# Kernel tuning notes

Hardware: AMD Instinct MI355X
Metric: run time of the kernel (lower is better)

Reference implementation:

```python
import jax, jax.numpy as jnp
import numpy as np

IN_FEATURES = 4096
OUT_FEATURES = 4096
CODESZ = 4
CB_SIZE = 256


def fwht(x):
    """Fast Walsh-Hadamard transform over the last dim (power of 2), unnormalized."""
    shape = x.shape
    n = shape[-1]
    x = x.reshape(-1, n)
    h = 1
    while h < n:  # log2(n) fixed iterations
        x = x.reshape(x.shape[0], -1, 2, h)
        a = x[:, :, 0:1, :]
        b = x[:, :, 1:2, :]
        x = jnp.concatenate([a + b, a - b], axis=2)
        h *= 2
    return x.reshape(shape)


def setup_inputs() -> dict:
    key = jax.random.key(0)
    k1, k2, k3, k4, k5, k6 = jax.random.split(key, 6)
    inp = {
        "input": jax.random.normal(k1, (4, 2048, IN_FEATURES), dtype=jnp.float32),
        "SU": jax.random.uniform(k2, (IN_FEATURES,), dtype=jnp.float32),
        "SV": jax.random.uniform(k3, (OUT_FEATURES,), dtype=jnp.float32),
        "cb": jax.random.normal(k4, (CB_SIZE, CODESZ), dtype=jnp.float32),
        "Qidxs": jax.random.randint(k5, (OUT_FEATURES, IN_FEATURES // CODESZ), 0, CB_SIZE, dtype=jnp.int32),
        "Wscale": jnp.ones((1,), dtype=jnp.float32),
        "bias": jax.random.normal(k6, (OUT_FEATURES,), dtype=jnp.float32),
    }
    return inp


def reference(input, SU, SV, cb, Qidxs, Wscale, bias):
    q_in = IN_FEATURES   # power of 2 -> had_left is None, K_left = 1
    q_out = OUT_FEATURES # power of 2 -> had_right is None, K_right = 1
    x = input.reshape(-1, input.shape[-1])          # [T, in]
    x = x * SU                                       # input sign/scale vector
    # matmul_hadUt_cuda: FWHT / sqrt(n) * wscale
    x = fwht(x) * (Wscale[0] / jnp.sqrt(jnp.float32(q_in)))
    # codebook decode + matmul: W [q_out, q_in] from indices
    W = cb[Qidxs].reshape(q_out, q_in)               # gather decode
    out = jnp.einsum('ti,oi->to', x, W)              # [T, q_out]
    # matmul_hadU_cuda on the output side: FWHT / sqrt(n)
    out = fwht(out) / jnp.sqrt(jnp.float32(q_out))
    out = out[..., :OUT_FEATURES]
    out = out * SV
    out = out.reshape(*input.shape[:-1], OUT_FEATURES)
    out = out + bias
    return out
```

## Files before the change

### kernel.cpp

```cpp
#include <hip/hip_runtime.h>
#include <cstdint>


using bf16x8 = __attribute__((ext_vector_type(8))) __bf16;
using f32x4  = __attribute__((ext_vector_type(4))) float;

__device__ __forceinline__ unsigned short f2bf(float f) {
    unsigned int u = __float_as_uint(f);
    unsigned int r = (u + 0x7fffu + ((u >> 16) & 1u)) >> 16;
    return (unsigned short)r;
}

__device__ __forceinline__ void h16(float v[16]) {
#pragma unroll
    for (int h = 1; h < 16; h <<= 1) {
#pragma unroll
        for (int g = 0; g < 16; g += (h << 1)) {
#pragma unroll
            for (int k = g; k < g + h; ++k) {
                float x = v[k], y = v[k + h];
                v[k] = x + y; v[k + h] = x - y;
            }
        }
    }
}


__global__ __launch_bounds__(256) void fwht_in_kernel(const float* __restrict__ inp,
                                                      const float* __restrict__ SU,
                                                      const float* __restrict__ wscale,
                                                      unsigned short* __restrict__ X) {
    __shared__ float s[4096];
    const int t = threadIdx.x;
    const size_t base = (size_t)blockIdx.x * 4096;
    const float4* in4 = (const float4*)(inp + base);
    const float4* su4 = (const float4*)SU;
#pragma unroll
    for (int j = 0; j < 4; ++j) {
        const int v = t + (j << 8);
        float4 x = in4[v];
        float4 u = su4[v];
        x.x *= u.x; x.y *= u.y; x.z *= u.z; x.w *= u.w;
        const int a = v >> 6, b = (v >> 2) & 15, c0 = (v & 3) << 2;
        float* row = s + a * 256 + ((b ^ a) << 4);
        row[(c0 + 0) ^ b] = x.x; row[(c0 + 1) ^ b] = x.y;
        row[(c0 + 2) ^ b] = x.z; row[(c0 + 3) ^ b] = x.w;
    }
    __syncthreads();
    float v[16];
    {
        const int a = t >> 4, b = t & 15;
        float* row = s + a * 256 + ((b ^ a) << 4);
#pragma unroll
        for (int c = 0; c < 16; ++c) v[c] = row[c ^ b];
        h16(v);
#pragma unroll
        for (int c = 0; c < 16; ++c) row[c ^ b] = v[c];
    }
    __syncthreads();
    {
        const int a = t >> 4, c = t & 15;
#pragma unroll
        for (int b = 0; b < 16; ++b) v[b] = s[a * 256 + ((b ^ a) << 4) + (c ^ b)];
        h16(v);
#pragma unroll
        for (int b = 0; b < 16; ++b) s[a * 256 + ((b ^ a) << 4) + (c ^ b)] = v[b];
    }
    __syncthreads();
    {
        const int b = t >> 4, c = t & 15;
#pragma unroll
        for (int a = 0; a < 16; ++a) v[a] = s[a * 256 + ((b ^ a) << 4) + (c ^ b)];
        h16(v);
#pragma unroll
        for (int a = 0; a < 16; ++a) s[a * 256 + ((b ^ a) << 4) + (c ^ b)] = v[a];
    }
    __syncthreads();
    const float sc = wscale[0] * 0.015625f;
#pragma unroll
    for (int p = 0; p < 2; ++p) {
        const int i0 = (p << 11) + (t << 3);
        const int a = i0 >> 8, b = (i0 >> 4) & 15, c0 = i0 & 15;
        const float* row = s + a * 256 + ((b ^ a) << 4);
        union { unsigned short us[8]; uint4 q; } pk;
#pragma unroll
        for (int z = 0; z < 8; ++z) pk.us[z] = f2bf(row[(c0 + z) ^ b] * sc);
        *(uint4*)(X + base + i0) = pk.q;
    }
}

__global__ __launch_bounds__(256) void decode_kernel(const int* __restrict__ Qidxs,
                                                     const float* __restrict__ cb,
                                                     unsigned short* __restrict__ Wb) {
    __shared__ float4 cbs[256];
    const int t = threadIdx.x;
    cbs[t] = ((const float4*)cb)[t];
    __syncthreads();
    const size_t o = blockIdx.x;
    const int* q = Qidxs + o * 1024;
    ushort4* wrow = (ushort4*)(Wb + o * 4096);
#pragma unroll
    for (int jj = 0; jj < 4; ++jj) {
        int j = t + (jj << 8);
        int idx = q[j];
        float4 v = cbs[idx];
        ushort4 w4;
        w4.x = f2bf(v.x); w4.y = f2bf(v.y); w4.z = f2bf(v.z); w4.w = f2bf(v.w);
        wrow[j] = w4;
    }
}


__device__ __forceinline__ void stage_part(const unsigned short* __restrict__ src,
                                           int grow, int kt,
                                           unsigned short* dst, int tid) {
#pragma unroll
    for (int j = 0; j < 2; ++j) {
        int u = tid + j * 512;
        int r = u >> 3;
        int q = (u & 7) ^ (r & 7);
        const unsigned short* g = src + (size_t)(grow + r) * 4096 + kt + q * 8;
        __builtin_amdgcn_global_load_lds(
            (const __attribute__((address_space(1))) unsigned int*)g,
            (__attribute__((address_space(3))) unsigned int*)((char*)dst + u * 16),
            16, 0, 0);
    }
}

#define VM4 asm volatile("s_waitcnt vmcnt(4)" ::: "memory")
#define VM0 asm volatile("s_waitcnt vmcnt(0)" ::: "memory")

#define RD_A(HOFF) do { _Pragma("unroll")                                          \
    for (int m_ = 0; m_ < 4; ++m_) {                                               \
        Ak0[m_] = *(const bf16x8*)(pA_ + (HOFF) + aRow + m_ * 4096 + pu0);         \
        Ak1[m_] = *(const bf16x8*)(pA_ + (HOFF) + aRow + m_ * 4096 + pu1);         \
    } } while (0)

#define RD_B(D0, D1, HOFF) do { _Pragma("unroll")                                  \
    for (int n_ = 0; n_ < 2; ++n_) {                                               \
        D0[n_] = *(const bf16x8*)(pB_ + (HOFF) + bRow + n_ * 8192 + pu0);          \
        D1[n_] = *(const bf16x8*)(pB_ + (HOFF) + bRow + n_ * 8192 + pu1);          \
    } } while (0)

#define MMQ(MQ, NQ, Bk0, Bk1) do {                                                 \
    __builtin_amdgcn_s_setprio(1);                                                 \
    _Pragma("unroll")                                                              \
    for (int m_ = 0; m_ < 4; ++m_) { _Pragma("unroll")                             \
        for (int n_ = 0; n_ < 2; ++n_) {                                           \
            acc[(MQ)*4+m_][(NQ)*2+n_] = __builtin_amdgcn_mfma_f32_16x16x32_bf16(   \
                Ak0[m_], Bk0[n_], acc[(MQ)*4+m_][(NQ)*2+n_], 0, 0, 0);             \
            acc[(MQ)*4+m_][(NQ)*2+n_] = __builtin_amdgcn_mfma_f32_16x16x32_bf16(   \
                Ak1[m_], Bk1[n_], acc[(MQ)*4+m_][(NQ)*2+n_], 0, 0, 0);             \
        } }                                                                        \
    __builtin_amdgcn_s_setprio(0); } while (0)

#define KTILE(PA, PB, ST1, ST2, ST3, ST4, VM_) do {                                \
    const char* pA_ = (const char*)(PA);                                           \
    const char* pB_ = (const char*)(PB);                                           \
    bf16x8 Ak0[4], Ak1[4], B0k0[2], B0k1[2], B1k0[2], B1k1[2];                     \
    RD_A(0); RD_B(B0k0, B0k1, 0); ST1; __builtin_amdgcn_s_barrier();               \
    MMQ(0, 0, B0k0, B0k1); __builtin_amdgcn_s_barrier();                           \
    RD_B(B1k0, B1k1, 16384); ST2; __builtin_amdgcn_s_barrier();                    \
    MMQ(0, 1, B1k0, B1k1); __builtin_amdgcn_s_barrier();                           \
    RD_A(16384); ST3; __builtin_amdgcn_s_barrier();                                \
    MMQ(1, 1, B1k0, B1k1); __builtin_amdgcn_s_barrier();                           \
    ST4; __builtin_amdgcn_s_barrier();                                             \
    MMQ(1, 0, B0k0, B0k1); VM_; __builtin_amdgcn_s_barrier();                      \
} while (0)

__global__ __launch_bounds__(512, 2) void gemm8_kernel(const unsigned short* __restrict__ X,
                                                       const unsigned short* __restrict__ Wb,
                                                       float* __restrict__ C) {
    __shared__ unsigned short ldsA[2][2][8192];
    __shared__ unsigned short ldsB[2][2][8192];

    const int tid  = threadIdx.x;
    const int lane = tid & 63;
    const int w    = tid >> 6;
    const int wm   = w >> 2;
    const int wn   = w & 3;

    const int bid   = blockIdx.x;
    const int xcd   = bid & 7;
    const int local = bid >> 3;
    const int tm = (xcd >> 1) * 8 + (local >> 3);
    const int tn = (xcd & 1) * 8 + (local & 7);
    const int brow = tm * 256;
    const int bcol = tn * 256;

    const int lr = lane & 15;
    const int lh = lane & 7;
    const int lg = lane >> 4;
    const int aRow = (wm * 16 + lr) * 128;
    const int bRow = (wn * 16 + lr) * 128;
    const int pu0 = (lg ^ lh) * 16;
    const int pu1 = ((4 + lg) ^ lh) * 16;

    f32x4 acc[8][4] = {};

    stage_part(X,  brow,       0,  &ldsA[0][0][0], tid);
    stage_part(Wb, bcol,       0,  &ldsB[0][0][0], tid);
    stage_part(Wb, bcol + 128, 0,  &ldsB[0][1][0], tid);
    stage_part(X,  brow + 128, 0,  &ldsA[0][1][0], tid);
    stage_part(X,  brow,       64, &ldsA[1][0][0], tid);
    stage_part(Wb, bcol,       64, &ldsB[1][0][0], tid);
    VM4;
    __builtin_amdgcn_s_barrier();

    for (int i = 0; i < 31; ++i) {
        const int kt1 = i * 128 + 64;
        const int ktA = i * 128 + 128;
        const int ktB = i * 128 + 192;
        KTILE(&ldsA[0][0][0], &ldsB[0][0][0],
              stage_part(Wb, bcol + 128, kt1, &ldsB[1][1][0], tid),
              stage_part(X,  brow + 128, kt1, &ldsA[1][1][0], tid),
              stage_part(X,  brow,       ktA, &ldsA[0][0][0], tid),
              stage_part(Wb, bcol,       ktA, &ldsB[0][0][0], tid), VM4);
        KTILE(&ldsA[1][0][0], &ldsB[1][0][0],
              stage_part(Wb, bcol + 128, ktA, &ldsB[0][1][0], tid),
              stage_part(X,  brow + 128, ktA, &ldsA[0][1][0], tid),
              stage_part(X,  brow,       ktB, &ldsA[1][0][0], tid),
              stage_part(Wb, bcol,       ktB, &ldsB[1][0][0], tid), VM4);
    }
    {
        const int kt1 = 31 * 128 + 64;
        KTILE(&ldsA[0][0][0], &ldsB[0][0][0],
              stage_part(Wb, bcol + 128, kt1, &ldsB[1][1][0], tid),
              stage_part(X,  brow + 128, kt1, &ldsA[1][1][0], tid),
              , , VM0);
        KTILE(&ldsA[1][0][0], &ldsB[1][0][0], , , , , );
    }

#pragma unroll
    for (int mf = 0; mf < 8; ++mf) {
        int row0 = brow + wm * 16 + mf * 32 + (lane >> 4) * 4;
#pragma unroll
        for (int nf = 0; nf < 4; ++nf) {
            int col = bcol + wn * 16 + nf * 64 + lr;
#pragma unroll
            for (int r = 0; r < 4; ++r)
                C[(size_t)(row0 + r) * 4096 + col] = acc[mf][nf][r];
        }
    }
}

__global__ __launch_bounds__(256) void fwht_out_kernel(float* __restrict__ out,
                                                       const float* __restrict__ SV,
                                                       const float* __restrict__ bias) {
    __shared__ float s[4096];
    const int t = threadIdx.x;
    const size_t base = (size_t)blockIdx.x * 4096;
    float4* o4 = (float4*)(out + base);
#pragma unroll
    for (int j = 0; j < 4; ++j) {
        const int v = t + (j << 8);
        float4 x = o4[v];
        const int a = v >> 6, b = (v >> 2) & 15, c0 = (v & 3) << 2;
        float* row = s + a * 256 + ((b ^ a) << 4);
        row[(c0 + 0) ^ b] = x.x; row[(c0 + 1) ^ b] = x.y;
        row[(c0 + 2) ^ b] = x.z; row[(c0 + 3) ^ b] = x.w;
    }
    __syncthreads();
    float v[16];
    {
        const int a = t >> 4, b = t & 15;
        float* row = s + a * 256 + ((b ^ a) << 4);
#pragma unroll
        for (int c = 0; c < 16; ++c) v[c] = row[c ^ b];
        h16(v);
#pragma unroll
        for (int c = 0; c < 16; ++c) row[c ^ b] = v[c];
    }
    __syncthreads();
    {
        const int a = t >> 4, c = t & 15;
#pragma unroll
        for (int b = 0; b < 16; ++b) v[b] = s[a * 256 + ((b ^ a) << 4) + (c ^ b)];
        h16(v);
#pragma unroll
        for (int b = 0; b < 16; ++b) s[a * 256 + ((b ^ a) << 4) + (c ^ b)] = v[b];
    }
    __syncthreads();
    {
        const int b = t >> 4, c = t & 15;
#pragma unroll
        for (int a = 0; a < 16; ++a) v[a] = s[a * 256 + ((b ^ a) << 4) + (c ^ b)];
        h16(v);
#pragma unroll
        for (int a = 0; a < 16; ++a) s[a * 256 + ((b ^ a) << 4) + (c ^ b)] = v[a];
    }
    __syncthreads();
    const float4* sv4 = (const float4*)SV;
    const float4* b4  = (const float4*)bias;
#pragma unroll
    for (int j = 0; j < 4; ++j) {
        const int vv = t + (j << 8);
        const int a = vv >> 6, b = (vv >> 2) & 15, c0 = (vv & 3) << 2;
        const float* row = s + a * 256 + ((b ^ a) << 4);
        float4 x;
        x.x = row[(c0 + 0) ^ b]; x.y = row[(c0 + 1) ^ b];
        x.z = row[(c0 + 2) ^ b]; x.w = row[(c0 + 3) ^ b];
        float4 sv = sv4[vv], bb = b4[vv];
        x.x = x.x * (sv.x * 0.015625f) + bb.x;
        x.y = x.y * (sv.y * 0.015625f) + bb.y;
        x.z = x.z * (sv.z * 0.015625f) + bb.z;
        x.w = x.w * (sv.w * 0.015625f) + bb.w;
        o4[vv] = x;
    }
}

extern "C" void kernel_launch(void* const* d_in, const int* in_sizes, int n_in,
                              void* d_out, int out_size, void* d_ws, size_t ws_size,
                              hipStream_t stream) {
    const float* inp    = (const float*)d_in[0];
    const float* SU     = (const float*)d_in[1];
    const float* SV     = (const float*)d_in[2];
    const float* cb     = (const float*)d_in[3];
    const int*   Qidxs  = (const int*)d_in[4];
    const float* Wscale = (const float*)d_in[5];
    const float* bias   = (const float*)d_in[6];
    float* out = (float*)d_out;

    unsigned short* X  = (unsigned short*)d_ws;
    unsigned short* Wb = (unsigned short*)((char*)d_ws + (size_t)8192 * 4096 * 2);

    hipLaunchKernelGGL(fwht_in_kernel, dim3(8192), dim3(256), 0, stream, inp, SU, Wscale, X);
    hipLaunchKernelGGL(decode_kernel,  dim3(4096), dim3(256), 0, stream, Qidxs, cb, Wb);
    hipLaunchKernelGGL(gemm8_kernel,   dim3(512),  dim3(512), 0, stream, X, Wb, out);
    hipLaunchKernelGGL(fwht_out_kernel, dim3(8192), dim3(256), 0, stream, out, SV, bias);
}
```

Baseline: 507.1 us.

## Fold output Hadamard into decoded weights and fuse SV/bias into GEMM epilogue

Uses linearity to apply the output-side FWHT to the decoded weight matrix along the output dimension (W' = H·W) once, inside a new decode kernel that works on 8-column slabs in shared memory. This removes the separate fwht_out pass over the 8192x4096 fp32 output, which was a full read-modify-write of the output. The SV scaling and bias add move into the GEMM store epilogue. Costs: the weight decode now does a 4096-point transform per column slab using a large LDS buffer (~147 KB), and bf16 rounding now happens after the transform instead of on the raw codebook values.

```diff
diff --git a/kernel.cpp b/kernel.cpp
--- a/kernel.cpp
+++ b/kernel.cpp
@@ -24,7 +24,6 @@
         }
     }
 }
-
 
 __global__ __launch_bounds__(256) void fwht_in_kernel(const float* __restrict__ inp,
                                                       const float* __restrict__ SU,
@@ -89,24 +88,77 @@
     }
 }
 
-__global__ __launch_bounds__(256) void decode_kernel(const int* __restrict__ Qidxs,
-                                                     const float* __restrict__ cb,
-                                                     unsigned short* __restrict__ Wb) {
+__global__ __launch_bounds__(512) void wfwht_kernel(const int* __restrict__ Qidxs,
+                                                    const float* __restrict__ cb,
+                                                    unsigned short* __restrict__ Wp) {
+    __shared__ float s[4096 * 9];
     __shared__ float4 cbs[256];
     const int t = threadIdx.x;
-    cbs[t] = ((const float4*)cb)[t];
-    __syncthreads();
-    const size_t o = blockIdx.x;
-    const int* q = Qidxs + o * 1024;
-    ushort4* wrow = (ushort4*)(Wb + o * 4096);
-#pragma unroll
-    for (int jj = 0; jj < 4; ++jj) {
-        int j = t + (jj << 8);
-        int idx = q[j];
-        float4 v = cbs[idx];
-        ushort4 w4;
-        w4.x = f2bf(v.x); w4.y = f2bf(v.y); w4.z = f2bf(v.z); w4.w = f2bf(v.w);
-        wrow[j] = w4;
+    const int bid = blockIdx.x;
+    const int p = (bid & 7) * 64 + (bid >> 3);
+    if (t < 256) cbs[t] = ((const float4*)cb)[t];
+    int idxs[16];
+#pragma unroll
+    for (int r = 0; r < 16; ++r) {
+        int task = t + (r << 9);
+        int o = task >> 1, j = task & 1;
+        idxs[r] = Qidxs[(size_t)o * 1024 + p * 2 + j];
+    }
+    __syncthreads();
+#pragma unroll
+    for (int r = 0; r < 16; ++r) {
+        int task = t + (r << 9);
+        int o = task >> 1, j = task & 1;
+        float4 v4 = cbs[idxs[r]];
+        float* row = s + o * 9 + j * 4;
+        row[0] = v4.x; row[1] = v4.y; row[2] = v4.z; row[3] = v4.w;
+    }
+    __syncthreads();
+    float v[16];
+#pragma unroll
+    for (int r = 0; r < 4; ++r) {
+        int tau = t + (r << 9);
+        int c = tau & 7, b = (tau >> 3) & 15, a = tau >> 7;
+        float* base = s + (a * 256 + b * 16) * 9 + c;
+#pragma unroll
+        for (int k = 0; k < 16; ++k) v[k] = base[k * 9];
+        h16(v);
+#pragma unroll
+        for (int k = 0; k < 16; ++k) base[k * 9] = v[k];
+    }
+    __syncthreads();
+#pragma unroll
+    for (int r = 0; r < 4; ++r) {
+        int tau = t + (r << 9);
+        int c = tau & 7, k = (tau >> 3) & 15, a = tau >> 7;
+        float* base = s + (a * 256 + k) * 9 + c;
+#pragma unroll
+        for (int m = 0; m < 16; ++m) v[m] = base[m * 144];
+        h16(v);
+#pragma unroll
+        for (int m = 0; m < 16; ++m) base[m * 144] = v[m];
+    }
+    __syncthreads();
+#pragma unroll
+    for (int r = 0; r < 4; ++r) {
+        int tau = t + (r << 9);
+        int c = tau & 7, k = (tau >> 3) & 15, b = tau >> 7;
+        float* base = s + (b * 16 + k) * 9 + c;
+#pragma unroll
+        for (int m = 0; m < 16; ++m) v[m] = base[m * 2304];
+        h16(v);
+#pragma unroll
+        for (int m = 0; m < 16; ++m) base[m * 2304] = v[m];
+    }
+    __syncthreads();
+#pragma unroll
+    for (int r = 0; r < 8; ++r) {
+        int o = t + (r << 9);
+        const float* row = s + o * 9;
+        union { unsigned short us[8]; uint4 q; } pk;
+#pragma unroll
+        for (int z = 0; z < 8; ++z) pk.us[z] = f2bf(row[z]);
+        *(uint4*)(Wp + (size_t)o * 4096 + p * 8) = pk.q;
     }
 }
 
@@ -170,7 +222,9 @@
 
 __global__ __launch_bounds__(512, 2) void gemm8_kernel(const unsigned short* __restrict__ X,
                                                        const unsigned short* __restrict__ Wb,
-                                                       float* __restrict__ C) {
+                                                       const float* __restrict__ SV,
+                                                       const float* __restrict__ bias,
+                                                       float* __restrict__ out) {
     __shared__ unsigned short ldsA[2][2][8192];
     __shared__ unsigned short ldsB[2][2][8192];
 
@@ -237,75 +291,12 @@
 #pragma unroll
         for (int nf = 0; nf < 4; ++nf) {
             int col = bcol + wn * 16 + nf * 64 + lr;
+            float sv = SV[col] * 0.015625f;
+            float bb = bias[col];
 #pragma unroll
             for (int r = 0; r < 4; ++r)
-                C[(size_t)(row0 + r) * 4096 + col] = acc[mf][nf][r];
+                out[(size_t)(row0 + r) * 4096 + col] = acc[mf][nf][r] * sv + bb;
         }
-    }
-}
-
-__global__ __launch_bounds__(256) void fwht_out_kernel(float* __restrict__ out,
-                                                       const float* __restrict__ SV,
-                                                       const float* __restrict__ bias) {
-    __shared__ float s[4096];
-    const int t = threadIdx.x;
-    const size_t base = (size_t)blockIdx.x * 4096;
-    float4* o4 = (float4*)(out + base);
-#pragma unroll
-    for (int j = 0; j < 4; ++j) {
-        const int v = t + (j << 8);
-        float4 x = o4[v];
-        const int a = v >> 6, b = (v >> 2) & 15, c0 = (v & 3) << 2;
-        float* row = s + a * 256 + ((b ^ a) << 4);
-        row[(c0 + 0) ^ b] = x.x; row[(c0 + 1) ^ b] = x.y;
-        row[(c0 + 2) ^ b] = x.z; row[(c0 + 3) ^ b] = x.w;
-    }
-    __syncthreads();
-    float v[16];
-    {
-        const int a = t >> 4, b = t & 15;
-        float* row = s + a * 256 + ((b ^ a) << 4);
-#pragma unroll
-        for (int c = 0; c < 16; ++c) v[c] = row[c ^ b];
-        h16(v);
-#pragma unroll
-        for (int c = 0; c < 16; ++c) row[c ^ b] = v[c];
-    }
-    __syncthreads();
-    {
-        const int a = t >> 4, c = t & 15;
-#pragma unroll
-        for (int b = 0; b < 16; ++b) v[b] = s[a * 256 + ((b ^ a) << 4) + (c ^ b)];
-        h16(v);
-#pragma unroll
-        for (int b = 0; b < 16; ++b) s[a * 256 + ((b ^ a) << 4) + (c ^ b)] = v[b];
-    }
-    __syncthreads();
-    {
-        const int b = t >> 4, c = t & 15;
-#pragma unroll
-        for (int a = 0; a < 16; ++a) v[a] = s[a * 256 + ((b ^ a) << 4) + (c ^ b)];
-        h16(v);
-#pragma unroll
-        for (int a = 0; a < 16; ++a) s[a * 256 + ((b ^ a) << 4) + (c ^ b)] = v[a];
-    }
-    __syncthreads();
-    const float4* sv4 = (const float4*)SV;
-    const float4* b4  = (const float4*)bias;
-#pragma unroll
-    for (int j = 0; j < 4; ++j) {
-        const int vv = t + (j << 8);
-        const int a = vv >> 6, b = (vv >> 2) & 15, c0 = (vv & 3) << 2;
-        const float* row = s + a * 256 + ((b ^ a) << 4);
-        float4 x;
-        x.x = row[(c0 + 0) ^ b]; x.y = row[(c0 + 1) ^ b];
-        x.z = row[(c0 + 2) ^ b]; x.w = row[(c0 + 3) ^ b];
-        float4 sv = sv4[vv], bb = b4[vv];
-        x.x = x.x * (sv.x * 0.015625f) + bb.x;
-        x.y = x.y * (sv.y * 0.015625f) + bb.y;
-        x.z = x.z * (sv.z * 0.015625f) + bb.z;
-        x.w = x.w * (sv.w * 0.015625f) + bb.w;
-        o4[vv] = x;
     }
 }
 
@@ -322,10 +313,9 @@
     float* out = (float*)d_out;
 
     unsigned short* X  = (unsigned short*)d_ws;
-    unsigned short* Wb = (unsigned short*)((char*)d_ws + (size_t)8192 * 4096 * 2);
+    unsigned short* Wp = (unsigned short*)((char*)d_ws + (size_t)8192 * 4096 * 2);
 
     hipLaunchKernelGGL(fwht_in_kernel, dim3(8192), dim3(256), 0, stream, inp, SU, Wscale, X);
-    hipLaunchKernelGGL(decode_kernel,  dim3(4096), dim3(256), 0, stream, Qidxs, cb, Wb);
-    hipLaunchKernelGGL(gemm8_kernel,   dim3(512),  dim3(512), 0, stream, X, Wb, out);
-    hipLaunchKernelGGL(fwht_out_kernel, dim3(8192), dim3(256), 0, stream, out, SV, bias);
-}
+    hipLaunchKernelGGL(wfwht_kernel,   dim3(512),  dim3(512), 0, stream, Qidxs, cb, Wp);
+    hipLaunchKernelGGL(gemm8_kernel,   dim3(512),  dim3(512), 0, stream, X, Wp, SV, bias, out);
+}
```

After: 497.5 us. About the same (-1.9%).
